# Kernel tuning notes

Measured on AMD Instinct MI355X. Metric: run time of the kernel, lower is better.

The kernel has to match this reference:

```python
import jax, jax.numpy as jnp
import numpy as np

NX, NY = 1024, 1024
N_VALUES = 64
N_CLASSES = 16
TEMPERATURE = 1.0  # forward() default
EPS = 1e-10


def setup_inputs() -> dict:
    key = jax.random.key(0)
    ks = jax.random.split(key, 5)
    x = jnp.linspace(0.0, 1.0, NX, dtype=jnp.float32)
    y = jnp.linspace(0.0, 1.0, NY, dtype=jnp.float32)
    gx, gy = jnp.meshgrid(x, y, indexing='ij')  # [NX,NY]
    return {
        'x_pos': gx.reshape(-1),                                   # [B]
        'y_pos': gy.reshape(-1),                                   # [B]
        'split_points': jax.random.uniform(ks[0], (N_VALUES,), jnp.float32) * 0.6 + 0.2,
        'split_directions_logits': jax.random.normal(ks[1], (N_VALUES,), jnp.float32),
        'class_logits': jax.random.normal(ks[2], (N_VALUES, N_CLASSES), jnp.float32),
        'child_selection_logits': jax.random.normal(ks[3], (N_VALUES, 2, N_VALUES), jnp.float32),
        'max_depth': 10,
    }


def reference(x_pos, y_pos, split_points, split_directions_logits, class_logits,
              child_selection_logits, max_depth):
    B = x_pos.shape[0]
    N = split_points.shape[0]
    t = TEMPERATURE
    dirs = jax.nn.sigmoid(split_directions_logits)                 # [N]
    # Per-point, per-node left split probability (constant over depth).
    h_left = jax.nn.sigmoid((split_points[None, :] - x_pos[:, None]) / t)  # [B,N]
    v_left = jax.nn.sigmoid((split_points[None, :] - y_pos[:, None]) / t)  # [B,N]
    left = (1.0 - dirs) * h_left + dirs * v_left                   # [B,N]
    # Node -> child routing matrices.
    L = jax.nn.softmax(child_selection_logits[:, 0, :] / t, axis=-1)  # [N,N]
    R = jax.nn.softmax(child_selection_logits[:, 1, :] / t, axis=-1)  # [N,N]

    p0 = jnp.zeros((B, N), dtype=x_pos.dtype).at[:, 0].set(1.0)

    def step(p, _):
        nxt = (p * left) @ L + (p * (1.0 - left)) @ R              # [B,N]
        nxt = nxt / jnp.clip(jnp.sum(nxt, axis=-1, keepdims=True), EPS)
        return nxt, None

    p, _ = jax.lax.scan(step, p0, None, length=int(max_depth))
    class_probs = p @ jax.nn.softmax(class_logits, axis=1)         # [B,C]
    return class_probs.reshape(NX, NY, N_CLASSES)
```

## Files before the change

kernel.cpp:

```cpp
#include <hip/hip_runtime.h>

typedef float f32x4 __attribute__((ext_vector_type(4)));
typedef _Float16 f16x8 __attribute__((ext_vector_type(8)));
typedef __fp16 fp16x2 __attribute__((ext_vector_type(2)));
typedef int i32x4 __attribute__((ext_vector_type(4)));

__device__ __forceinline__ unsigned short f2h_bits(float f) {
    _Float16 h = (_Float16)f;
    return __builtin_bit_cast(unsigned short, h);
}
__device__ __forceinline__ float sigmoidf(float x) { return 1.0f / (1.0f + expf(-x)); }

__global__ void fractal_setup_a(const float* __restrict__ csl, const float* __restrict__ cls,
                                const float* __restrict__ sp, const float* __restrict__ sdl,
                                float* __restrict__ smg, float* __restrict__ csmg,
                                float* __restrict__ tbl) {
    const int tid = threadIdx.x;
    if (blockIdx.x < 32) {
        const int w = tid >> 6;
        const int lane = tid & 63;
        const int r = blockIdx.x * 4 + w;
        const int node = r & 63;
        const int side = r >> 6;
        const float v = csl[node * 128 + side * 64 + lane];
        float mx = v;
#pragma unroll
        for (int msk = 1; msk < 64; msk <<= 1) mx = fmaxf(mx, __shfl_xor(mx, msk, 64));
        const float e = expf(v - mx);
        float sum = e;
#pragma unroll
        for (int msk = 1; msk < 64; msk <<= 1) sum += __shfl_xor(sum, msk, 64);
        smg[r * 64 + lane] = e / sum;
    } else {
        if (tid < 64) {
            const float* rowp = cls + tid * 16;
            float mx = -1e30f;
            for (int j = 0; j < 16; ++j) mx = fmaxf(mx, rowp[j]);
            float ssum = 0.f;
            for (int j = 0; j < 16; ++j) ssum += expf(rowp[j] - mx);
            const float inv = 1.0f / ssum;
            for (int j = 0; j < 16; ++j) csmg[tid * 16 + j] = expf(rowp[j] - mx) * inv;
        } else if (tid >= 128 && tid < 192) {
            tbl[tid - 128] = expf(-sp[tid - 128]);
        } else if (tid >= 192) {
            tbl[64 + tid - 192] = sigmoidf(sdl[tid - 192]);
        }
    }
}

__global__ void fractal_setup_b(const float* __restrict__ smg, const float* __restrict__ csmg,
                                unsigned short* __restrict__ frag_out) {
    const int e = blockIdx.x * 256 + threadIdx.x;
    if (e < 8192) {
        const int j = e & 7;
        const int l = (e >> 3) & 63;
        const int fi = e >> 9;
        const int t = fi >> 2, c = fi & 3;
        const int i = l & 15;
        const int n = 8 * (i >> 2) + (i & 3) + 4 * (t & 1) + 32 * (t >> 1);
        const int k0 = (c & 1) * 32 + (l >> 4) * 8 + j;
        float v;
        if (c < 2) v = smg[(64 + k0) * 64 + n];
        else       v = smg[k0 * 64 + n] - smg[(64 + k0) * 64 + n];
        frag_out[e] = f2h_bits(v);
    } else {
        const int e2 = e - 8192;
        const int j = e2 & 7;
        const int l = (e2 >> 3) & 63;
        const int c = e2 >> 9;
        const int n = l & 15;
        const int k = c * 32 + (l >> 4) * 8 + j;
        frag_out[8192 + e2] = f2h_bits(csmg[k * 16 + n]);
    }
}

__device__ __forceinline__ void fractal_step(const f16x8 (&bfr)[4][4],
                                             const f16x8& lfA0, const f16x8& lfA1,
                                             const f16x8& lfB0, const f16x8& lfB1,
                                             i32x4& puA0, i32x4& puA1,
                                             i32x4& puB0, i32x4& puB1) {
    const f16x8 pfA0 = __builtin_bit_cast(f16x8, puA0);
    const f16x8 pfA1 = __builtin_bit_cast(f16x8, puA1);
    const f16x8 pfB0 = __builtin_bit_cast(f16x8, puB0);
    const f16x8 pfB1 = __builtin_bit_cast(f16x8, puB1);
    const f16x8 aA0 = pfA0 * lfA0;
    const f16x8 aA1 = pfA1 * lfA1;
    const f16x8 aB0 = pfB0 * lfB0;
    const f16x8 aB1 = pfB1 * lfB1;
    int PA[4], QA[4], PB[4], QB[4];
#pragma unroll
    for (int t = 0; t < 4; ++t) {
        f32x4 CA = {0.f, 0.f, 0.f, 0.f};
        f32x4 CB = {0.f, 0.f, 0.f, 0.f};
        CA = __builtin_amdgcn_mfma_f32_16x16x32_f16(bfr[t][0], pfA0, CA, 0, 0, 0);
        CB = __builtin_amdgcn_mfma_f32_16x16x32_f16(bfr[t][0], pfB0, CB, 0, 0, 0);
        CA = __builtin_amdgcn_mfma_f32_16x16x32_f16(bfr[t][1], pfA1, CA, 0, 0, 0);
        CB = __builtin_amdgcn_mfma_f32_16x16x32_f16(bfr[t][1], pfB1, CB, 0, 0, 0);
        CA = __builtin_amdgcn_mfma_f32_16x16x32_f16(bfr[t][2], aA0, CA, 0, 0, 0);
        CB = __builtin_amdgcn_mfma_f32_16x16x32_f16(bfr[t][2], aB0, CB, 0, 0, 0);
        CA = __builtin_amdgcn_mfma_f32_16x16x32_f16(bfr[t][3], aA1, CA, 0, 0, 0);
        CB = __builtin_amdgcn_mfma_f32_16x16x32_f16(bfr[t][3], aB1, CB, 0, 0, 0);
        PA[t] = __builtin_bit_cast(int, __builtin_amdgcn_cvt_pkrtz(CA[0], CA[1]));
        QA[t] = __builtin_bit_cast(int, __builtin_amdgcn_cvt_pkrtz(CA[2], CA[3]));
        PB[t] = __builtin_bit_cast(int, __builtin_amdgcn_cvt_pkrtz(CB[0], CB[1]));
        QB[t] = __builtin_bit_cast(int, __builtin_amdgcn_cvt_pkrtz(CB[2], CB[3]));
    }
    puA0.x = PA[0]; puA0.y = QA[0]; puA0.z = PA[1]; puA0.w = QA[1];
    puA1.x = PA[2]; puA1.y = QA[2]; puA1.z = PA[3]; puA1.w = QA[3];
    puB0.x = PB[0]; puB0.y = QB[0]; puB0.z = PB[1]; puB0.w = QB[1];
    puB1.x = PB[2]; puB1.y = QB[2]; puB1.z = PB[3]; puB1.w = QB[3];
}

__global__ __launch_bounds__(256, 2)
void fractal_main(const float* __restrict__ x_pos, const float* __restrict__ y_pos,
                  const int* __restrict__ mdp,
                  const unsigned short* __restrict__ frags,
                  const float* __restrict__ tbl,
                  float* __restrict__ out) {
    const int tid = threadIdx.x;
    const int w = tid >> 6;
    const int l = tid & 63;
    const int q = l >> 4;
    const int m = l & 15;
    const int rowbase = (blockIdx.x * 4 + w) * 32;

    const f16x8* __restrict__ fgp = (const f16x8*)frags;
    f16x8 bfr[4][4];
#pragma unroll
    for (int t = 0; t < 4; ++t)
#pragma unroll
        for (int c = 0; c < 4; ++c) bfr[t][c] = fgp[(t * 4 + c) * 64 + l];

    f32x4 tE0[2], tE1[2], tD0[2], tD1[2];
    tE0[0] = *(const f32x4*)(tbl + 8 * q);       tE0[1] = *(const f32x4*)(tbl + 8 * q + 4);
    tE1[0] = *(const f32x4*)(tbl + 32 + 8 * q);  tE1[1] = *(const f32x4*)(tbl + 32 + 8 * q + 4);
    tD0[0] = *(const f32x4*)(tbl + 64 + 8 * q);  tD0[1] = *(const f32x4*)(tbl + 64 + 8 * q + 4);
    tD1[0] = *(const f32x4*)(tbl + 96 + 8 * q);  tD1[1] = *(const f32x4*)(tbl + 96 + 8 * q + 4);

    const float xA = x_pos[rowbase + m],      yA = y_pos[rowbase + m];
    const float xB = x_pos[rowbase + 16 + m], yB = y_pos[rowbase + 16 + m];
    const float exA = __expf(xA), eyA = __expf(yA);
    const float exB = __expf(xB), eyB = __expf(yB);

    f16x8 lfA0, lfA1, lfB0, lfB1;
#pragma unroll
    for (int j = 0; j < 8; ++j) {
        const float E0 = tE0[j >> 2][j & 3];
        const float E1 = tE1[j >> 2][j & 3];
        const float d0 = tD0[j >> 2][j & 3];
        const float d1 = tD1[j >> 2][j & 3];
        {
            const float h0 = __builtin_amdgcn_rcpf(__builtin_fmaf(exA, E0, 1.0f));
            const float v0 = __builtin_amdgcn_rcpf(__builtin_fmaf(eyA, E0, 1.0f));
            const float h1 = __builtin_amdgcn_rcpf(__builtin_fmaf(exA, E1, 1.0f));
            const float v1 = __builtin_amdgcn_rcpf(__builtin_fmaf(eyA, E1, 1.0f));
            lfA0[j] = (_Float16)(h0 + d0 * (v0 - h0));
            lfA1[j] = (_Float16)(h1 + d1 * (v1 - h1));
        }
        {
            const float h0 = __builtin_amdgcn_rcpf(__builtin_fmaf(exB, E0, 1.0f));
            const float v0 = __builtin_amdgcn_rcpf(__builtin_fmaf(eyB, E0, 1.0f));
            const float h1 = __builtin_amdgcn_rcpf(__builtin_fmaf(exB, E1, 1.0f));
            const float v1 = __builtin_amdgcn_rcpf(__builtin_fmaf(eyB, E1, 1.0f));
            lfB0[j] = (_Float16)(h0 + d0 * (v0 - h0));
            lfB1[j] = (_Float16)(h1 + d1 * (v1 - h1));
        }
    }

    i32x4 puA0 = {0, 0, 0, 0}, puA1 = {0, 0, 0, 0};
    i32x4 puB0 = {0, 0, 0, 0}, puB1 = {0, 0, 0, 0};
    if (q == 0) { puA0.x = 0x3C00; puB0.x = 0x3C00; }

    const int md = mdp[0];
    if (md == 10) {
#pragma unroll
        for (int d = 0; d < 10; ++d)
            fractal_step(bfr, lfA0, lfA1, lfB0, lfB1, puA0, puA1, puB0, puB1);
    } else {
        for (int d = 0; d < md; ++d)
            fractal_step(bfr, lfA0, lfA1, lfB0, lfB1, puA0, puA1, puB0, puB1);
    }

    f16x8 bcs[2];
#pragma unroll
    for (int c = 0; c < 2; ++c) bcs[c] = fgp[1024 + c * 64 + l];

    {
        const f16x8 pf0 = __builtin_bit_cast(f16x8, puA0);
        const f16x8 pf1 = __builtin_bit_cast(f16x8, puA1);
        f32x4 o = {0.f, 0.f, 0.f, 0.f};
        o = __builtin_amdgcn_mfma_f32_16x16x32_f16(bcs[0], pf0, o, 0, 0, 0);
        o = __builtin_amdgcn_mfma_f32_16x16x32_f16(bcs[1], pf1, o, 0, 0, 0);
        float s = o[0] + o[1] + o[2] + o[3];
        s += __shfl_xor(s, 16, 64);
        s += __shfl_xor(s, 32, 64);
        const float inv = 1.0f / fmaxf(s, 1e-10f);
        f32x4 res;
#pragma unroll
        for (int r = 0; r < 4; ++r) res[r] = o[r] * inv;
        *(f32x4*)(out + (rowbase + m) * 16 + 4 * q) = res;
    }
    {
        const f16x8 pf0 = __builtin_bit_cast(f16x8, puB0);
        const f16x8 pf1 = __builtin_bit_cast(f16x8, puB1);
        f32x4 o = {0.f, 0.f, 0.f, 0.f};
        o = __builtin_amdgcn_mfma_f32_16x16x32_f16(bcs[0], pf0, o, 0, 0, 0);
        o = __builtin_amdgcn_mfma_f32_16x16x32_f16(bcs[1], pf1, o, 0, 0, 0);
        float s = o[0] + o[1] + o[2] + o[3];
        s += __shfl_xor(s, 16, 64);
        s += __shfl_xor(s, 32, 64);
        const float inv = 1.0f / fmaxf(s, 1e-10f);
        f32x4 res;
#pragma unroll
        for (int r = 0; r < 4; ++r) res[r] = o[r] * inv;
        *(f32x4*)(out + (rowbase + 16 + m) * 16 + 4 * q) = res;
    }
}

extern "C" void kernel_launch(void* const* d_in, const int* in_sizes, int n_in,
                              void* d_out, int out_size, void* d_ws, size_t ws_size,
                              hipStream_t stream) {
    const float* x_pos = (const float*)d_in[0];
    const float* y_pos = (const float*)d_in[1];
    const float* sp    = (const float*)d_in[2];
    const float* sdl   = (const float*)d_in[3];
    const float* cls   = (const float*)d_in[4];
    const float* csl   = (const float*)d_in[5];
    const int*   mdp   = (const int*)d_in[6];

    unsigned short* frags = (unsigned short*)d_ws;
    float* tbl  = (float*)((char*)d_ws + 18432);
    float* smg  = (float*)((char*)d_ws + 19456);
    float* csmg = (float*)((char*)d_ws + 52224);

    fractal_setup_a<<<33, 256, 0, stream>>>(csl, cls, sp, sdl, smg, csmg, tbl);
    fractal_setup_b<<<36, 256, 0, stream>>>(smg, csmg, frags);

    const int B = in_sizes[0];
    fractal_main<<<B / 128, 256, 0, stream>>>(x_pos, y_pos, mdp, frags, tbl,
                                              (float*)d_out);
}
```

Baseline: 194.9 us.

## Peel first and last routing steps into closed-form and fused class projection

```diff
diff --git a/kernel.cpp b/kernel.cpp
--- a/kernel.cpp
+++ b/kernel.cpp
@@ -2,7 +2,6 @@
 
 typedef float f32x4 __attribute__((ext_vector_type(4)));
 typedef _Float16 f16x8 __attribute__((ext_vector_type(8)));
-typedef __fp16 fp16x2 __attribute__((ext_vector_type(2)));
 typedef int i32x4 __attribute__((ext_vector_type(4)));
 
 __device__ __forceinline__ unsigned short f2h_bits(float f) {
@@ -49,7 +48,8 @@
 }
 
 __global__ void fractal_setup_b(const float* __restrict__ smg, const float* __restrict__ csmg,
-                                unsigned short* __restrict__ frag_out) {
+                                unsigned short* __restrict__ frag_out,
+                                float* __restrict__ row0) {
     const int e = blockIdx.x * 256 + threadIdx.x;
     if (e < 8192) {
         const int j = e & 7;
@@ -63,7 +63,7 @@
         if (c < 2) v = smg[(64 + k0) * 64 + n];
         else       v = smg[k0 * 64 + n] - smg[(64 + k0) * 64 + n];
         frag_out[e] = f2h_bits(v);
-    } else {
+    } else if (e < 9216) {
         const int e2 = e - 8192;
         const int j = e2 & 7;
         const int l = (e2 >> 3) & 63;
@@ -71,6 +71,27 @@
         const int n = l & 15;
         const int k = c * 32 + (l >> 4) * 8 + j;
         frag_out[8192 + e2] = f2h_bits(csmg[k * 16 + n]);
+    } else if (e < 11264) {
+        const int e3 = e - 9216;
+        const int f = e3 >> 9;
+        const int rem = e3 & 511;
+        const int j = rem & 7;
+        const int l = (rem >> 3) & 63;
+        const int cls = l & 15;
+        const int k = (f & 1) * 32 + ((l >> 4) << 3) + j;
+        float acc = 0.f;
+        if (f < 2) {
+            for (int n = 0; n < 64; ++n)
+                acc += smg[(64 + k) * 64 + n] * csmg[n * 16 + cls];
+        } else {
+            for (int n = 0; n < 64; ++n)
+                acc += (smg[k * 64 + n] - smg[(64 + k) * 64 + n]) * csmg[n * 16 + cls];
+        }
+        frag_out[9216 + e3] = f2h_bits(acc);
+    } else if (e < 11392) {
+        const int e2 = e - 11264;
+        row0[e2] = (e2 < 64) ? smg[4096 + e2]
+                             : (smg[e2 - 64] - smg[4096 + (e2 - 64)]);
     }
 }
 
@@ -116,6 +137,8 @@
                   const int* __restrict__ mdp,
                   const unsigned short* __restrict__ frags,
                   const float* __restrict__ tbl,
+                  const float* __restrict__ row0,
+                  const float* __restrict__ csmg,
                   float* __restrict__ out) {
     const int tid = threadIdx.x;
     const int w = tid >> 6;
@@ -123,6 +146,21 @@
     const int q = l >> 4;
     const int m = l & 15;
     const int rowbase = (blockIdx.x * 4 + w) * 32;
+
+    const int md = mdp[0];
+    if (md == 0) {
+        const f32x4 cv = *(const f32x4*)(csmg + 4 * q);
+        float s = cv[0] + cv[1] + cv[2] + cv[3];
+        s += __shfl_xor(s, 16, 64);
+        s += __shfl_xor(s, 32, 64);
+        const float inv = 1.0f / fmaxf(s, 1e-10f);
+        f32x4 res;
+#pragma unroll
+        for (int r = 0; r < 4; ++r) res[r] = cv[r] * inv;
+        *(f32x4*)(out + (rowbase + m) * 16 + 4 * q) = res;
+        *(f32x4*)(out + (rowbase + 16 + m) * 16 + 4 * q) = res;
+        return;
+    }
 
     const f16x8* __restrict__ fgp = (const f16x8*)frags;
     f16x8 bfr[4][4];
@@ -167,30 +205,69 @@
         }
     }
 
-    i32x4 puA0 = {0, 0, 0, 0}, puA1 = {0, 0, 0, 0};
-    i32x4 puB0 = {0, 0, 0, 0}, puB1 = {0, 0, 0, 0};
-    if (q == 0) { puA0.x = 0x3C00; puB0.x = 0x3C00; }
-
-    const int md = mdp[0];
-    if (md == 10) {
-#pragma unroll
-        for (int d = 0; d < 10; ++d)
-            fractal_step(bfr, lfA0, lfA1, lfB0, lfB1, puA0, puA1, puB0, puB1);
+    i32x4 puA0, puA1, puB0, puB1;
+    if (md >= 2) {
+        const float E00 = tbl[0];
+        const float dir0 = tbl[64];
+        float lA, lB;
+        {
+            const float h = __builtin_amdgcn_rcpf(__builtin_fmaf(exA, E00, 1.0f));
+            const float v = __builtin_amdgcn_rcpf(__builtin_fmaf(eyA, E00, 1.0f));
+            lA = h + dir0 * (v - h);
+        }
+        {
+            const float h = __builtin_amdgcn_rcpf(__builtin_fmaf(exB, E00, 1.0f));
+            const float v = __builtin_amdgcn_rcpf(__builtin_fmaf(eyB, E00, 1.0f));
+            lB = h + dir0 * (v - h);
+        }
+        f32x4 rRa[2], rRb[2], rDa[2], rDb[2];
+        rRa[0] = *(const f32x4*)(row0 + 8 * q);       rRa[1] = *(const f32x4*)(row0 + 8 * q + 4);
+        rRb[0] = *(const f32x4*)(row0 + 32 + 8 * q);  rRb[1] = *(const f32x4*)(row0 + 32 + 8 * q + 4);
+        rDa[0] = *(const f32x4*)(row0 + 64 + 8 * q);  rDa[1] = *(const f32x4*)(row0 + 64 + 8 * q + 4);
+        rDb[0] = *(const f32x4*)(row0 + 96 + 8 * q);  rDb[1] = *(const f32x4*)(row0 + 96 + 8 * q + 4);
+        f16x8 pA0, pA1, pB0, pB1;
+#pragma unroll
+        for (int j = 0; j < 8; ++j) {
+            const float R0 = rRa[j >> 2][j & 3], R1 = rRb[j >> 2][j & 3];
+            const float D0 = rDa[j >> 2][j & 3], D1 = rDb[j >> 2][j & 3];
+            pA0[j] = (_Float16)__builtin_fmaf(lA, D0, R0);
+            pA1[j] = (_Float16)__builtin_fmaf(lA, D1, R1);
+            pB0[j] = (_Float16)__builtin_fmaf(lB, D0, R0);
+            pB1[j] = (_Float16)__builtin_fmaf(lB, D1, R1);
+        }
+        puA0 = __builtin_bit_cast(i32x4, pA0);
+        puA1 = __builtin_bit_cast(i32x4, pA1);
+        puB0 = __builtin_bit_cast(i32x4, pB0);
+        puB1 = __builtin_bit_cast(i32x4, pB1);
+
+        if (md == 10) {
+#pragma unroll
+            for (int d = 0; d < 8; ++d)
+                fractal_step(bfr, lfA0, lfA1, lfB0, lfB1, puA0, puA1, puB0, puB1);
+        } else {
+            for (int d = 0; d < md - 2; ++d)
+                fractal_step(bfr, lfA0, lfA1, lfB0, lfB1, puA0, puA1, puB0, puB1);
+        }
     } else {
-        for (int d = 0; d < md; ++d)
-            fractal_step(bfr, lfA0, lfA1, lfB0, lfB1, puA0, puA1, puB0, puB1);
-    }
-
-    f16x8 bcs[2];
-#pragma unroll
-    for (int c = 0; c < 2; ++c) bcs[c] = fgp[1024 + c * 64 + l];
+        puA0 = (i32x4){0, 0, 0, 0}; puA1 = (i32x4){0, 0, 0, 0};
+        puB0 = (i32x4){0, 0, 0, 0}; puB1 = (i32x4){0, 0, 0, 0};
+        if (q == 0) { puA0.x = 0x3C00; puB0.x = 0x3C00; }
+    }
+
+    f16x8 bfin[4];
+#pragma unroll
+    for (int f = 0; f < 4; ++f) bfin[f] = fgp[1152 + f * 64 + l];
 
     {
         const f16x8 pf0 = __builtin_bit_cast(f16x8, puA0);
         const f16x8 pf1 = __builtin_bit_cast(f16x8, puA1);
+        const f16x8 a0 = pf0 * lfA0;
+        const f16x8 a1 = pf1 * lfA1;
         f32x4 o = {0.f, 0.f, 0.f, 0.f};
-        o = __builtin_amdgcn_mfma_f32_16x16x32_f16(bcs[0], pf0, o, 0, 0, 0);
-        o = __builtin_amdgcn_mfma_f32_16x16x32_f16(bcs[1], pf1, o, 0, 0, 0);
+        o = __builtin_amdgcn_mfma_f32_16x16x32_f16(bfin[0], pf0, o, 0, 0, 0);
+        o = __builtin_amdgcn_mfma_f32_16x16x32_f16(bfin[1], pf1, o, 0, 0, 0);
+        o = __builtin_amdgcn_mfma_f32_16x16x32_f16(bfin[2], a0, o, 0, 0, 0);
+        o = __builtin_amdgcn_mfma_f32_16x16x32_f16(bfin[3], a1, o, 0, 0, 0);
         float s = o[0] + o[1] + o[2] + o[3];
         s += __shfl_xor(s, 16, 64);
         s += __shfl_xor(s, 32, 64);
@@ -203,9 +280,13 @@
     {
         const f16x8 pf0 = __builtin_bit_cast(f16x8, puB0);
         const f16x8 pf1 = __builtin_bit_cast(f16x8, puB1);
+        const f16x8 a0 = pf0 * lfB0;
+        const f16x8 a1 = pf1 * lfB1;
         f32x4 o = {0.f, 0.f, 0.f, 0.f};
-        o = __builtin_amdgcn_mfma_f32_16x16x32_f16(bcs[0], pf0, o, 0, 0, 0);
-        o = __builtin_amdgcn_mfma_f32_16x16x32_f16(bcs[1], pf1, o, 0, 0, 0);
+        o = __builtin_amdgcn_mfma_f32_16x16x32_f16(bfin[0], pf0, o, 0, 0, 0);
+        o = __builtin_amdgcn_mfma_f32_16x16x32_f16(bfin[1], pf1, o, 0, 0, 0);
+        o = __builtin_amdgcn_mfma_f32_16x16x32_f16(bfin[2], a0, o, 0, 0, 0);
+        o = __builtin_amdgcn_mfma_f32_16x16x32_f16(bfin[3], a1, o, 0, 0, 0);
         float s = o[0] + o[1] + o[2] + o[3];
         s += __shfl_xor(s, 16, 64);
         s += __shfl_xor(s, 32, 64);
@@ -229,14 +310,15 @@
     const int*   mdp   = (const int*)d_in[6];
 
     unsigned short* frags = (unsigned short*)d_ws;
-    float* tbl  = (float*)((char*)d_ws + 18432);
-    float* smg  = (float*)((char*)d_ws + 19456);
-    float* csmg = (float*)((char*)d_ws + 52224);
+    float* tbl  = (float*)((char*)d_ws + 22528);
+    float* row0 = (float*)((char*)d_ws + 23040);
+    float* smg  = (float*)((char*)d_ws + 23552);
+    float* csmg = (float*)((char*)d_ws + 56320);
 
     fractal_setup_a<<<33, 256, 0, stream>>>(csl, cls, sp, sdl, smg, csmg, tbl);
-    fractal_setup_b<<<36, 256, 0, stream>>>(smg, csmg, frags);
+    fractal_setup_b<<<45, 256, 0, stream>>>(smg, csmg, frags, row0);
 
     const int B = in_sizes[0];
-    fractal_main<<<B / 128, 256, 0, stream>>>(x_pos, y_pos, mdp, frags, tbl,
-                                              (float*)d_out);
-}
+    fractal_main<<<B / 128, 256, 0, stream>>>(x_pos, y_pos, mdp, frags, tbl, row0,
+                                              csmg, (float*)d_out);
+}
```

Measured after the change: 189.1 us. -3.0%, faster.
